# Optimization experiments

Hardware: AMD Instinct MI355X
Metric: run time of the kernel (lower is better)

The kernel has to match this reference:

```python
import jax, jax.numpy as jnp
import numpy as np

K, N, M = 65536, 4096, 64  # observations, basis centers, features


def setup_inputs() -> dict:
    key = jax.random.key(0)
    k1, k2, k3, k4 = jax.random.split(key, 4)
    x = jax.random.normal(k1, (K, M), dtype=jnp.float32)
    x_basis = jax.random.normal(k2, (N, M), dtype=jnp.float32)
    w = jax.random.normal(k3, (1, N), dtype=jnp.float32) / np.sqrt(N)
    b = jax.random.normal(k4, (1,), dtype=jnp.float32)
    return {"x": x, "x_basis": x_basis, "w": w, "b": b}


def reference(x, x_basis, w, b):
    # pairwise squared distances ||x_i - c_j||^2, [K, N]
    x2 = jnp.sum(x * x, axis=1, keepdims=True)          # [K, 1]
    c2 = jnp.sum(x_basis * x_basis, axis=1)             # [N]
    sq = x2 + c2[None, :] - 2.0 * (x @ x_basis.T)       # [K, N]
    phi = jnp.exp(-sq)                                  # gaussian RBF
    return jax.nn.sigmoid(phi @ w.T + b)                # [K, 1]
```

## Files before the change

kernel.cpp:

```cpp
#include <hip/hip_runtime.h>


#define KOBS 65536
#define NCENT 4096
#define MFEAT 64

#define SCALE_A 2.8853900817779268f
#define QS      1.4426950408889634f
#define TSKIP   -60.0f

typedef __attribute__((ext_vector_type(4)))  float float4v;
typedef __attribute__((ext_vector_type(16))) float float16v;
typedef __attribute__((ext_vector_type(8)))  int   int8v;

#if __has_builtin(__builtin_amdgcn_exp2f)
#define EXP2F(x) __builtin_amdgcn_exp2f(x)
#else
#define EXP2F(x) exp2f(x)
#endif

static __device__ inline unsigned f2bfu(float f) {
    unsigned u = __float_as_uint(f);
    return (u + 0x7fffu + ((u >> 16) & 1u)) >> 16;
}

#define MFMA(A, B, C) __builtin_amdgcn_mfma_scale_f32_32x32x64_f8f6f4( \
    (A), (B), (C), 0, 0, 0, 0x7f7f7f7f, 0, 0x7f7f7f7f)

__global__ __launch_bounds__(256) void rbf_prep(
    const float* __restrict__ xb, const float* __restrict__ w,
    char* __restrict__ cb, unsigned* __restrict__ hcw) {
    const int bid = blockIdx.x;
    const int tid = threadIdx.x;
    if (bid < 128) {
        const int o      = bid * 256 + tid;
        const int col    = o >> 3;
        const int joct   = o & 7;
        const int c      = col >> 7;
        const int w4     = (col >> 5) & 3;
        const int lanelo = col & 31;
        const int l      = lanelo + (joct >> 2) * 32;
        const int j0     = (joct & 3) * 8;
        const float* src = xb + col * MFEAT + joct * 8;
        float4v v0 = *(const float4v*)(src);
        float4v v1 = *(const float4v*)(src + 4);
        int lo = __builtin_amdgcn_cvt_pk_fp8_f32(v0[0], v0[1], 0, false);
        lo     = __builtin_amdgcn_cvt_pk_fp8_f32(v0[2], v0[3], lo, true);
        int hi = __builtin_amdgcn_cvt_pk_fp8_f32(v1[0], v1[1], 0, false);
        hi     = __builtin_amdgcn_cvt_pk_fp8_f32(v1[2], v1[3], hi, true);
        unsigned long long pk = (unsigned long long)(unsigned)lo |
                                ((unsigned long long)(unsigned)hi << 32);
        *(unsigned long long*)(cb + (size_t)((c * 4 + w4) * 64 + l) * 32 + j0) = pk;
    } else {
        const int row  = (bid - 128) * 4 + (tid >> 6);
        const int lane = tid & 63;
        float v = xb[row * MFEAT + lane];
        float s = v * v;
        #pragma unroll
        for (int off = 32; off > 0; off >>= 1) s += __shfl_xor(s, off, 64);
        if (lane == 0)
            hcw[row] = (f2bfu(TSKIP + QS * s) << 16) | f2bfu(w[row]);
    }
}

__global__ __launch_bounds__(512, 8) void rbf_main(
    const float* __restrict__ x, const char* __restrict__ cb,
    const unsigned* __restrict__ hcw, const float* __restrict__ bptr,
    float* __restrict__ out) {
    __shared__ float x2s[64];
    __shared__ float zl[64];

    const int tid  = threadIdx.x;
    const int wv   = tid >> 6;
    const int lane = tid & 63;
    const int ll   = lane & 31;
    const int lh   = lane >> 5;
    const int rt   = wv >> 2;
    const int wq   = wv & 3;
    const int bid  = (int)blockIdx.x;
    const int rt32 = rt * 32;
    const int rb   = 4 * lh;

    if (tid < 64) zl[tid] = 0.0f;

    int8v af;
    {
        const float* xr = x + (size_t)(bid * 64 + rt32 + ll) * MFEAT + lh * 32;
        float ss = 0.0f;
        #pragma unroll
        for (int rg = 0; rg < 8; ++rg) {
            float4v v = *(const float4v*)(xr + rg * 4);
            ss = fmaf(v[0], v[0], ss); ss = fmaf(v[1], v[1], ss);
            ss = fmaf(v[2], v[2], ss); ss = fmaf(v[3], v[3], ss);
            int pk = __builtin_amdgcn_cvt_pk_fp8_f32(
                SCALE_A * v[0], SCALE_A * v[1], 0, false);
            pk = __builtin_amdgcn_cvt_pk_fp8_f32(
                SCALE_A * v[2], SCALE_A * v[3], pk, true);
            af[rg] = pk;
        }
        ss += __shfl_xor(ss, 32, 64);
        if (wq == 0 && lh == 0) x2s[rt32 + ll] = ss;
    }
    __syncthreads();

    float pmx;
    {
        float pv = x2s[rt32 + ll];
        pv = fminf(pv, __shfl_xor(pv, 1,  64));
        pv = fminf(pv, __shfl_xor(pv, 2,  64));
        pv = fminf(pv, __shfl_xor(pv, 4,  64));
        pv = fminf(pv, __shfl_xor(pv, 8,  64));
        pv = fminf(pv, __shfl_xor(pv, 16, 64));
        pmx = -QS * pv;
    }

    const unsigned cboff = (unsigned)(wq * 64 + lane) * 32u;
    const unsigned moff  = (unsigned)(wq * 32 + ll);

    int8v    pb[2];
    unsigned mw[2];

    #define LOADB(C, S) do {                                               \
        pb[S] = *(const int8v*)(cb + cboff + (unsigned)(C) * 8192u);       \
        mw[S] = hcw[moff + (unsigned)(C) * 128u];                          \
    } while (0)

    #define STEP(C, S, DOLOAD) do {                                       \
        const unsigned mu = mw[S];                                        \
        const float tq  = __uint_as_float(mu & 0xffff0000u);              \
        const float wv_ = __uint_as_float(mu << 16);                      \
        float16v d;                                                       \
        _Pragma("unroll")                                                 \
        for (int z_ = 0; z_ < 16; ++z_) d[z_] = 0.0f;                     \
        d = MFMA(af, pb[S], d);                                           \
        if (DOLOAD) LOADB((C) + 2, S);                                    \
        float u0 = fmaxf(fmaxf(d[0],  d[1]),  d[2]);                      \
        float u1 = fmaxf(fmaxf(d[3],  d[4]),  d[5]);                      \
        float u2 = fmaxf(fmaxf(d[6],  d[7]),  d[8]);                      \
        float u3 = fmaxf(fmaxf(d[9],  d[10]), d[11]);                     \
        float u4 = fmaxf(fmaxf(d[12], d[13]), d[14]);                     \
        float mxd = fmaxf(fmaxf(fmaxf(u0, u1), u2),                       \
                          fmaxf(fmaxf(u3, u4), d[15]));                   \
        const float thr = tq - pmx;              \
        if (__any(mxd > thr)) {                       \
            const float q = TSKIP - tq;             \
            if (mxd > thr) {                                              \
                _Pragma("unroll")                                         \
                for (int i_ = 0; i_ < 16; ++i_) {                         \
                    const int row_ = rb + (i_ & 3) + 8 * (i_ >> 2);       \
                    const float pi_ = -QS * x2s[rt32 + row_];             \
                    atomicAdd(&zl[rt32 + row_],                           \
                              wv_ * EXP2F(d[i_] + pi_ + q));              \
                }                                                         \
            }                                                             \
        }                                                                 \
    } while (0)

    LOADB(0, 0);
    LOADB(1, 1);

    #pragma unroll 1
    for (int c = 0; c < 30; c += 2) {
        STEP(c,     0, 1);
        STEP(c + 1, 1, 1);
    }
    STEP(30, 0, 0);
    STEP(31, 1, 0);

    #undef STEP
    #undef LOADB

    __syncthreads();
    if (tid < 64) {
        const float z = zl[tid] + bptr[0];
        out[bid * 64 + tid] = 1.0f / (1.0f + EXP2F(-QS * z));
    }
}

extern "C" void kernel_launch(void* const* d_in, const int* in_sizes, int n_in,
                              void* d_out, int out_size, void* d_ws, size_t ws_size,
                              hipStream_t stream) {
    const float* x  = (const float*)d_in[0];
    const float* xb = (const float*)d_in[1];
    const float* w  = (const float*)d_in[2];
    const float* b  = (const float*)d_in[3];
    float* out = (float*)d_out;

    char*     cb  = (char*)d_ws;
    unsigned* hcw = (unsigned*)((char*)d_ws + NCENT * MFEAT);

    rbf_prep<<<128 + NCENT / 4, 256, 0, stream>>>(xb, w, cb, hcw);
    rbf_main<<<KOBS / 64, 512, 0, stream>>>(x, cb, hcw, b, out);
}
```

Before: 104.8 us.

## Fold row norms into MFMA accumulator, tighten skip test, halve block size

Result: faster. 96.44 us (-8.0%).

```diff
diff --git a/kernel.cpp b/kernel.cpp
--- a/kernel.cpp
+++ b/kernel.cpp
@@ -4,6 +4,7 @@
 #define KOBS 65536
 #define NCENT 4096
 #define MFEAT 64
+#define NCHUNK 32
 
 #define SCALE_A 2.8853900817779268f
 #define QS      1.4426950408889634f
@@ -26,6 +27,16 @@
 
 #define MFMA(A, B, C) __builtin_amdgcn_mfma_scale_f32_32x32x64_f8f6f4( \
     (A), (B), (C), 0, 0, 0, 0x7f7f7f7f, 0, 0x7f7f7f7f)
+
+#define MAX16(DST, AV) do {                                        \
+    float t0_ = fmaxf(fmaxf((AV)[0],  (AV)[1]),  (AV)[2]);         \
+    float t1_ = fmaxf(fmaxf((AV)[3],  (AV)[4]),  (AV)[5]);         \
+    float t2_ = fmaxf(fmaxf((AV)[6],  (AV)[7]),  (AV)[8]);         \
+    float t3_ = fmaxf(fmaxf((AV)[9],  (AV)[10]), (AV)[11]);        \
+    float t4_ = fmaxf(fmaxf((AV)[12], (AV)[13]), (AV)[14]);        \
+    DST = fmaxf(fmaxf(fmaxf(t0_, t1_), t2_),                       \
+                fmaxf(fmaxf(t3_, t4_), (AV)[15]));                 \
+} while (0)
 
 __global__ __launch_bounds__(256) void rbf_prep(
     const float* __restrict__ xb, const float* __restrict__ w,
@@ -63,29 +74,26 @@
     }
 }
 
-__global__ __launch_bounds__(512, 8) void rbf_main(
+__global__ __launch_bounds__(256, 6) void rbf_main(
     const float* __restrict__ x, const char* __restrict__ cb,
     const unsigned* __restrict__ hcw, const float* __restrict__ bptr,
     float* __restrict__ out) {
-    __shared__ float x2s[64];
-    __shared__ float zl[64];
+    __shared__ float x2s[32];
+    __shared__ float zl[32];
 
     const int tid  = threadIdx.x;
-    const int wv   = tid >> 6;
+    const int wq   = tid >> 6;
     const int lane = tid & 63;
     const int ll   = lane & 31;
     const int lh   = lane >> 5;
-    const int rt   = wv >> 2;
-    const int wq   = wv & 3;
     const int bid  = (int)blockIdx.x;
-    const int rt32 = rt * 32;
     const int rb   = 4 * lh;
 
-    if (tid < 64) zl[tid] = 0.0f;
+    if (tid < 32) zl[tid] = 0.0f;
 
     int8v af;
     {
-        const float* xr = x + (size_t)(bid * 64 + rt32 + ll) * MFEAT + lh * 32;
+        const float* xr = x + (size_t)(bid * 32 + ll) * MFEAT + lh * 32;
         float ss = 0.0f;
         #pragma unroll
         for (int rg = 0; rg < 8; ++rg) {
@@ -99,81 +107,59 @@
             af[rg] = pk;
         }
         ss += __shfl_xor(ss, 32, 64);
-        if (wq == 0 && lh == 0) x2s[rt32 + ll] = ss;
+        if (wq == 0 && lh == 0) x2s[ll] = ss;
     }
     __syncthreads();
 
-    float pmx;
-    {
-        float pv = x2s[rt32 + ll];
-        pv = fminf(pv, __shfl_xor(pv, 1,  64));
-        pv = fminf(pv, __shfl_xor(pv, 2,  64));
-        pv = fminf(pv, __shfl_xor(pv, 4,  64));
-        pv = fminf(pv, __shfl_xor(pv, 8,  64));
-        pv = fminf(pv, __shfl_xor(pv, 16, 64));
-        pmx = -QS * pv;
-    }
+    float16v p;
+    #pragma unroll
+    for (int i = 0; i < 16; ++i)
+        p[i] = -QS * x2s[rb + (i & 3) + 8 * (i >> 2)];
 
     const unsigned cboff = (unsigned)(wq * 64 + lane) * 32u;
     const unsigned moff  = (unsigned)(wq * 32 + ll);
 
-    int8v    pb[2];
-    unsigned mw[2];
+    int8v    pb0, pb1;
+    unsigned mw0, mw1;
 
-    #define LOADB(C, S) do {                                               \
-        pb[S] = *(const int8v*)(cb + cboff + (unsigned)(C) * 8192u);       \
-        mw[S] = hcw[moff + (unsigned)(C) * 128u];                          \
+    pb0 = *(const int8v*)(cb + cboff);
+    mw0 = hcw[moff];
+    pb1 = *(const int8v*)(cb + cboff + 8192u);
+    mw1 = hcw[moff + 128u];
+
+    #define STEP(C, PB, MW) do {                                           \
+        const float tq  = __uint_as_float(MW & 0xffff0000u);               \
+        const float wv_ = __uint_as_float(MW << 16);                       \
+        float16v d = MFMA(af, PB, p);                                      \
+        if ((C) + 2 < NCHUNK) {                                            \
+            PB = *(const int8v*)(cb + cboff + (unsigned)((C) + 2) * 8192u);\
+            MW = hcw[moff + (unsigned)((C) + 2) * 128u];                   \
+        }                                                                  \
+        float mx;                                                          \
+        MAX16(mx, d);                                                      \
+        if (__any(mx > tq)) {                    \
+            if (mx > tq) {                                                 \
+                const float q = TSKIP - tq;          \
+                _Pragma("unroll")                                          \
+                for (int i_ = 0; i_ < 16; ++i_)                            \
+                    atomicAdd(&zl[rb + (i_ & 3) + 8 * (i_ >> 2)],          \
+                              wv_ * EXP2F(d[i_] + q));                     \
+            }                                                              \
+        }                                                                  \
     } while (0)
 
-    #define STEP(C, S, DOLOAD) do {                                       \
-        const unsigned mu = mw[S];                                        \
-        const float tq  = __uint_as_float(mu & 0xffff0000u);              \
-        const float wv_ = __uint_as_float(mu << 16);                      \
-        float16v d;                                                       \
-        _Pragma("unroll")                                                 \
-        for (int z_ = 0; z_ < 16; ++z_) d[z_] = 0.0f;                     \
-        d = MFMA(af, pb[S], d);                                           \
-        if (DOLOAD) LOADB((C) + 2, S);                                    \
-        float u0 = fmaxf(fmaxf(d[0],  d[1]),  d[2]);                      \
-        float u1 = fmaxf(fmaxf(d[3],  d[4]),  d[5]);                      \
-        float u2 = fmaxf(fmaxf(d[6],  d[7]),  d[8]);                      \
-        float u3 = fmaxf(fmaxf(d[9],  d[10]), d[11]);                     \
-        float u4 = fmaxf(fmaxf(d[12], d[13]), d[14]);                     \
-        float mxd = fmaxf(fmaxf(fmaxf(u0, u1), u2),                       \
-                          fmaxf(fmaxf(u3, u4), d[15]));                   \
-        const float thr = tq - pmx;              \
-        if (__any(mxd > thr)) {                       \
-            const float q = TSKIP - tq;             \
-            if (mxd > thr) {                                              \
-                _Pragma("unroll")                                         \
-                for (int i_ = 0; i_ < 16; ++i_) {                         \
-                    const int row_ = rb + (i_ & 3) + 8 * (i_ >> 2);       \
-                    const float pi_ = -QS * x2s[rt32 + row_];             \
-                    atomicAdd(&zl[rt32 + row_],                           \
-                              wv_ * EXP2F(d[i_] + pi_ + q));              \
-                }                                                         \
-            }                                                             \
-        }                                                                 \
-    } while (0)
-
-    LOADB(0, 0);
-    LOADB(1, 1);
-
     #pragma unroll 1
-    for (int c = 0; c < 30; c += 2) {
-        STEP(c,     0, 1);
-        STEP(c + 1, 1, 1);
+    for (int c = 0; c < NCHUNK; c += 2) {
+        STEP(c,     pb0, mw0);
+        STEP(c + 1, pb1, mw1);
     }
-    STEP(30, 0, 0);
-    STEP(31, 1, 0);
 
     #undef STEP
-    #undef LOADB
 
     __syncthreads();
-    if (tid < 64) {
+    if (tid < 32) {
         const float z = zl[tid] + bptr[0];
-        out[bid * 64 + tid] = 1.0f / (1.0f + EXP2F(-QS * z));
+        out[bid * 32 + tid] = 1.0f / (1.0f + EXP2F(-QS * z));
     }
 }
 
@@ -190,5 +176,5 @@
     unsigned* hcw = (unsigned*)((char*)d_ws + NCENT * MFEAT);
 
     rbf_prep<<<128 + NCENT / 4, 256, 0, stream>>>(xb, w, cb, hcw);
-    rbf_main<<<KOBS / 64, 512, 0, stream>>>(x, cb, hcw, b, out);
+    rbf_main<<<KOBS / 32, 256, 0, stream>>>(x, cb, hcw, b, out);
 }
```
